# Kernel tuning notes

Hardware: AMD Instinct MI355X
Metric: run time of the kernel (lower is better)

## Reference

```python
import jax, jax.numpy as jnp
import numpy as np

N = 50000        # nodes
E = 800000       # edges (before self-loops)
IN = 128         # in_dim
H = 2            # heads
C1 = 64          # hidden_dim (per head)
D1 = H * C1      # conv1 concat output = 128
OUT = 64         # out_dim
C2 = 2 * OUT     # conv2 per-head channels = 128 (concat=False -> mean over heads)
NEG = 0.2        # GATv2 leaky_relu negative slope
EPS = 1e-5       # BatchNorm eps


def setup_inputs() -> dict:
    key = jax.random.key(0)
    ks = jax.random.split(key, 14)
    s = 0.05
    inp = {
        "x": jax.random.normal(ks[0], (N, IN), jnp.float32),
        "edge_index": jax.random.randint(ks[1], (2, E), 0, N, dtype=jnp.int32),
        # conv1 (GATv2: lin_l for source, lin_r for target, att vector per head)
        "W_l1": jax.random.normal(ks[2], (IN, D1), jnp.float32) * s,
        "b_l1": jnp.zeros((D1,), jnp.float32),
        "W_r1": jax.random.normal(ks[3], (IN, D1), jnp.float32) * s,
        "b_r1": jnp.zeros((D1,), jnp.float32),
        "att1": jax.random.normal(ks[4], (H, C1), jnp.float32) * s,
        "bias1": jnp.zeros((D1,), jnp.float32),
        # batch_norm1 (affine)
        "gamma1": jnp.ones((D1,), jnp.float32),
        "beta1": jnp.zeros((D1,), jnp.float32),
        # conv2
        "W_l2": jax.random.normal(ks[5], (D1, H * C2), jnp.float32) * s,
        "b_l2": jnp.zeros((H * C2,), jnp.float32),
        "W_r2": jax.random.normal(ks[6], (D1, H * C2), jnp.float32) * s,
        "b_r2": jnp.zeros((H * C2,), jnp.float32),
        "att2": jax.random.normal(ks[7], (H, C2), jnp.float32) * s,
        "bias2": jnp.zeros((C2,), jnp.float32),
    }
    return inp


def gatv2_layer(x, src, dst, W_l, b_l, W_r, b_r, att, bias, concat):
    Hh, Cc = att.shape
    x_l = (x @ W_l + b_l).reshape(N, Hh, Cc)   # source transform
    x_r = (x @ W_r + b_r).reshape(N, Hh, Cc)   # target transform
    # per-edge GATv2 score: att . leaky_relu(x_l[j] + x_r[i])
    e = jax.nn.leaky_relu(x_l[src] + x_r[dst], NEG)      # [E', H, C]
    logit = jnp.einsum("ehc,hc->eh", e, att)              # [E', H]
    # segment softmax over incoming edges of each target node
    m = jax.ops.segment_max(logit, dst, num_segments=N)   # [N, H]
    ex = jnp.exp(logit - m[dst])
    den = jax.ops.segment_sum(ex, dst, num_segments=N)    # [N, H]
    alpha = ex / den[dst]                                  # [E', H]
    out = jax.ops.segment_sum(x_l[src] * alpha[:, :, None], dst, num_segments=N)
    out = out.reshape(N, Hh * Cc) if concat else out.mean(axis=1)
    return out + bias


def batchnorm(x, gamma=None, beta=None):
    mu = x.mean(axis=0)
    var = x.var(axis=0)  # biased variance, as used by BN for normalization
    xn = (x - mu) * jax.lax.rsqrt(var + EPS)
    if gamma is not None:
        xn = xn * gamma + beta
    return xn


def reference(x, edge_index, W_l1, b_l1, W_r1, b_r1, att1, bias1, gamma1, beta1,
              W_l2, b_l2, W_r2, b_r2, att2, bias2):
    loops = jnp.arange(N, dtype=edge_index.dtype)
    src = jnp.concatenate([edge_index[0], loops])  # add self-loops (PyG default)
    dst = jnp.concatenate([edge_index[1], loops])
    h = gatv2_layer(x, src, dst, W_l1, b_l1, W_r1, b_r1, att1, bias1, True)
    h = jax.nn.relu(batchnorm(h, gamma1, beta1))
    o = gatv2_layer(h, src, dst, W_l2, b_l2, W_r2, b_r2, att2, bias2, False)
    mu_part = batchnorm(o[:, :OUT])                      # affine=False
    return jnp.concatenate([mu_part, jax.nn.softplus(o[:, OUT:])], axis=1)
```

## Files before the change

kernel.cpp:

```cpp
#include <hip/hip_runtime.h>
#include <hip/hip_bf16.h>
#include <math.h>

#define NNODES 50000
#define NEDGES 800000
#define EPTOT  (NEDGES + NNODES)
#define NEG_SLOPE 0.2f
#define BN_EPS 1e-5f
#define LOG2E 1.44269504088896f
#define ESLOT 64

#define PB_W1  128
#define PB_W2  (PB_W1 + 256)
#define GEMM1_GX 392
#define SCAT_BX  3321

typedef __hip_bfloat16 bf16;
typedef __attribute__((ext_vector_type(8))) short short8;
typedef __attribute__((ext_vector_type(4))) float f32x4;
typedef __attribute__((ext_vector_type(2))) float f32x2;

__device__ __forceinline__ unsigned short f2us(float f){
    return (unsigned short)(__bfloat16_as_ushort(__float2bfloat16(f)));
}
__device__ __forceinline__ f32x2 unpk(unsigned int w){
    union { unsigned int u; float f; } lo, hi;
    lo.u = w << 16; hi.u = w & 0xffff0000u;
    f32x2 r; r.x = lo.f; r.y = hi.f; return r;
}
__device__ __forceinline__ f32x2 pkmax(f32x2 a, f32x2 b){
#if __has_builtin(__builtin_elementwise_max)
    return __builtin_elementwise_max(a, b);
#else
    f32x2 r; r.x = fmaxf(a.x, b.x); r.y = fmaxf(a.y, b.y); return r;
#endif
}
__device__ __forceinline__ unsigned int pack2(float a, float b){
    return (unsigned int)f2us(a) | ((unsigned int)f2us(b) << 16);
}

template<int CTRL>
__device__ __forceinline__ float dppadd(float v){
    int p = __builtin_amdgcn_update_dpp(0, __float_as_int(v), CTRL, 0xf, 0xf, true);
    return v + __int_as_float(p);
}
template<int G>
__device__ __forceinline__ float group_sum(float v){
    if constexpr (G == 16){
        v = dppadd<0x121>(v);
        v = dppadd<0x122>(v);
        v = dppadd<0x124>(v);
        v = dppadd<0x128>(v);
    } else {
        v = dppadd<0xB1>(v);
        v = dppadd<0x4E>(v);
        v += __shfl_xor(v, 4, 64);
    }
    return v;
}


__global__ __launch_bounds__(256) void misc_prep(
    const float* __restrict__ Wl1, const float* __restrict__ Wr1,
    const float* __restrict__ bl1, const float* __restrict__ br1,
    bf16* __restrict__ WT1, float* __restrict__ bc1,
    const float* __restrict__ Wl2, const float* __restrict__ Wr2,
    const float* __restrict__ bl2, const float* __restrict__ br2,
    bf16* __restrict__ WT2, float* __restrict__ bc2)
{
    int b = blockIdx.x;
    if (b < PB_W1){
        int i = b * 256 + threadIdx.x;
        int r = i >> 7, k = i & 127;
        const float* W = (r < 128) ? Wl1 : Wr1;
        int c = (r < 128) ? r : r - 128;
        WT1[i] = __float2bfloat16(W[k * 128 + c]);
        if (k == 0) bc1[r] = (r < 128) ? bl1[c] : br1[c];
    } else {
        int i = (b - PB_W1) * 256 + threadIdx.x;
        int r = i >> 7, k = i & 127;
        const float* W = (r < 256) ? Wl2 : Wr2;
        int c = (r < 256) ? r : r - 256;
        WT2[i] = __float2bfloat16(W[k * 256 + c]);
        if (k == 0) bc2[r] = (r < 256) ? bl2[c] : br2[c];
    }
}


template<int DTOT, int AMODE, int NT, bool SCATTER>
__global__ __launch_bounds__(128) void mfma_gemm(
    const void* __restrict__ A, const bf16* __restrict__ WT,
    const float* __restrict__ biascat,
    bf16* __restrict__ xl, bf16* __restrict__ xr,
    const float* __restrict__ bns, const float* __restrict__ gamma,
    const float* __restrict__ beta,
    const int* __restrict__ ei, int* __restrict__ cnt, int* __restrict__ esrc)
{
    if (SCATTER && blockIdx.x >= GEMM1_GX){
        int e = ((blockIdx.x - GEMM1_GX) * 2 + blockIdx.y) * 128 + threadIdx.x;
        if (e < EPTOT){
            int s, d;
            if (e < NEDGES){ s = ei[e]; d = ei[NEDGES + e]; } else { s = d = e - NEDGES; }
            int pos = atomicAdd(&cnt[d], 1);
            if (pos < ESLOT) esrc[(d << 6) + pos] = s;
        }
        return;
    }

    int wave = threadIdx.x >> 6;
    int lane = threadIdx.x & 63;
    int quad = lane >> 4;
    int l16  = lane & 15;
    int m0 = blockIdx.x * 128 + wave * 64;
    const float* Af = (const float*)A;
    const unsigned int* Ao = (const unsigned int*)A;
    const short* Bp = (const short*)WT;

    short8 af[4][4];
    #pragma unroll
    for (int k = 0; k < 4; ++k){
        float sc[8], sh[8];
        if (AMODE == 2){
            const float inv_n = 1.f / (float)NNODES;
            int cb = k * 32 + quad * 8;
            #pragma unroll
            for (int j = 0; j < 8; ++j){
                float mu = bns[cb + j] * inv_n;
                float s  = gamma[cb + j] * rsqrtf(bns[128 + cb + j] * inv_n - mu * mu + BN_EPS);
                sc[j] = s; sh[j] = beta[cb + j] - mu * s;
            }
        }
        #pragma unroll
        for (int mt = 0; mt < 4; ++mt){
            int m = m0 + mt * 16 + l16;
            m = (m < NNODES) ? m : (NNODES - 1);
            if (AMODE == 1){
                float4 v0 = *(const float4*)(Af + (size_t)m * 128 + k * 32 + quad * 8);
                float4 v1 = *(const float4*)(Af + (size_t)m * 128 + k * 32 + quad * 8 + 4);
                unsigned int* u = (unsigned int*)&af[k][mt];
                u[0] = pack2(v0.x, v0.y); u[1] = pack2(v0.z, v0.w);
                u[2] = pack2(v1.x, v1.y); u[3] = pack2(v1.z, v1.w);
            } else {
                uint4 w = *(const uint4*)(Ao + (size_t)m * 64 + k * 16 + quad * 4);
                f32x2 v0 = unpk(w.x), v1 = unpk(w.y), v2 = unpk(w.z), v3 = unpk(w.w);
                float f0 = v0.x * sc[0] + sh[0], f1 = v0.y * sc[1] + sh[1];
                float f2 = v1.x * sc[2] + sh[2], f3 = v1.y * sc[3] + sh[3];
                float f4 = v2.x * sc[4] + sh[4], f5 = v2.y * sc[5] + sh[5];
                float f6 = v3.x * sc[6] + sh[6], f7 = v3.y * sc[7] + sh[7];
                f0 = f0 > 0.f ? f0 : 0.f; f1 = f1 > 0.f ? f1 : 0.f;
                f2 = f2 > 0.f ? f2 : 0.f; f3 = f3 > 0.f ? f3 : 0.f;
                f4 = f4 > 0.f ? f4 : 0.f; f5 = f5 > 0.f ? f5 : 0.f;
                f6 = f6 > 0.f ? f6 : 0.f; f7 = f7 > 0.f ? f7 : 0.f;
                unsigned int* u = (unsigned int*)&af[k][mt];
                u[0] = pack2(f0, f1); u[1] = pack2(f2, f3);
                u[2] = pack2(f4, f5); u[3] = pack2(f6, f7);
            }
        }
    }

    for (int t = 0; t < NT; ++t){
        int n0 = (blockIdx.y * NT + t) * 64;
        f32x4 acc[4][4] = {};
        #pragma unroll
        for (int k = 0; k < 4; ++k){
            short8 bfr[4];
            #pragma unroll
            for (int nt = 0; nt < 4; ++nt){
                int n = n0 + nt * 16 + l16;
                bfr[nt] = *(const short8*)(Bp + (size_t)n * 128 + k * 32 + quad * 8);
            }
            #pragma unroll
            for (int mt = 0; mt < 4; ++mt)
                #pragma unroll
                for (int nt = 0; nt < 4; ++nt)
                    acc[mt][nt] = __builtin_amdgcn_mfma_f32_16x16x32_bf16(af[k][mt], bfr[nt], acc[mt][nt], 0, 0, 0);
        }
        #pragma unroll
        for (int nt = 0; nt < 4; ++nt){
            int n = n0 + nt * 16 + l16;
            float bi = biascat[n];
            bf16* outp = (n < DTOT) ? xl : xr;
            int c = (n < DTOT) ? n : n - DTOT;
            #pragma unroll
            for (int mt = 0; mt < 4; ++mt)
                #pragma unroll
                for (int r = 0; r < 4; ++r){
                    int m = m0 + mt * 16 + quad * 4 + r;
                    if (m < NNODES)
                        outp[(size_t)m * DTOT + c] = __float2bfloat16(acc[mt][nt][r] + bi);
                }
        }
    }
}


template<int C, bool MEAN>
__global__ __launch_bounds__(256) void gat_aggregate(
    const bf16* __restrict__ xl, const bf16* __restrict__ xr,
    const float* __restrict__ att, const int* __restrict__ cnt,
    const int* __restrict__ esrc, void* __restrict__ outv,
    const float* __restrict__ bias2)
{
    constexpr int GH  = C / 8;
    constexpr int LPE = 2 * GH;
    constexpr int EL  = 64 / LPE;
    constexpr int RB  = 4 * C;
    int lane = threadIdx.x & 63;
    int wave = threadIdx.x >> 6;
    int n    = blockIdx.x * 4 + wave;
    int el   = lane / LPE;
    int h    = (lane / GH) & 1;
    int cl   = lane % GH;
    int rowoff = h * (C * 2) + cl * 16;
    const char* xlp = (const char*)xl;

    int srcAll = esrc[(n << 6) + lane];
    int cc = cnt[n];
    int c = (cc < ESLOT) ? cc : ESLOT;
    uint4 xw = *(const uint4*)((const char*)xr + (unsigned)n * RB + rowoff);
    f32x2 xr0 = unpk(xw.x), xr1 = unpk(xw.y), xr2v = unpk(xw.z), xr3 = unpk(xw.w);
    const float* ap = att + h * C + cl * 8;
    f32x2 av0 = {ap[0] * LOG2E, ap[1] * LOG2E};
    f32x2 av1 = {ap[2] * LOG2E, ap[3] * LOG2E};
    f32x2 av2 = {ap[4] * LOG2E, ap[5] * LOG2E};
    f32x2 av3 = {ap[6] * LOG2E, ap[7] * LOG2E};
    float b2r[8];
    if (MEAN){
        #pragma unroll
        for (int v = 0; v < 8; ++v) b2r[v] = bias2[cl * 8 + v];
    }

    float den = 0.f;
    f32x2 a0 = {0.f,0.f}, a1 = {0.f,0.f}, a2 = {0.f,0.f}, a3 = {0.f,0.f};

    int i0 = el, i1 = EL + el;
    int sa = __shfl(srcAll, (i0 < c) ? i0 : (c - 1), 64);
    int sb = __shfl(srcAll, (i1 < c) ? i1 : (c - 1), 64);
    uint4 wa = *(const uint4*)(xlp + ((unsigned)sa * (unsigned)RB + rowoff));
    uint4 wb = *(const uint4*)(xlp + ((unsigned)sb * (unsigned)RB + rowoff));

    int p = 0;
    for (; p + EL < c; p += 2 * EL){
        float mkb = (p + EL + el < c) ? 0.f : -1e30f;
        int pn = p + 2 * EL;
        uint4 wa_n, wb_n;
        bool pf = pn < c;
        if (pf){
            int ian = pn + el, ibn = pn + EL + el;
            int sa_n = __shfl(srcAll, (ian < c) ? ian : (c - 1), 64);
            int sb_n = __shfl(srcAll, (ibn < c) ? ibn : (c - 1), 64);
            wa_n = *(const uint4*)(xlp + ((unsigned)sa_n * (unsigned)RB + rowoff));
            wb_n = *(const uint4*)(xlp + ((unsigned)sb_n * (unsigned)RB + rowoff));
        }

        f32x2 xa0 = unpk(wa.x), xa1 = unpk(wa.y), xa2 = unpk(wa.z), xa3 = unpk(wa.w);
        f32x2 xb0 = unpk(wb.x), xb1 = unpk(wb.y), xb2 = unpk(wb.z), xb3 = unpk(wb.w);

        f32x2 ua0 = xa0 + xr0, ua1 = xa1 + xr1, ua2 = xa2 + xr2v, ua3 = xa3 + xr3;
        f32x2 ub0 = xb0 + xr0, ub1 = xb1 + xr1, ub2 = xb2 + xr2v, ub3 = xb3 + xr3;

        f32x2 ppa = pkmax(ua0, ua0 * NEG_SLOPE) * av0;
        ppa += pkmax(ua1, ua1 * NEG_SLOPE) * av1;
        ppa += pkmax(ua2, ua2 * NEG_SLOPE) * av2;
        ppa += pkmax(ua3, ua3 * NEG_SLOPE) * av3;
        f32x2 ppb = pkmax(ub0, ub0 * NEG_SLOPE) * av0;
        ppb += pkmax(ub1, ub1 * NEG_SLOPE) * av1;
        ppb += pkmax(ub2, ub2 * NEG_SLOPE) * av2;
        ppb += pkmax(ub3, ub3 * NEG_SLOPE) * av3;
        float parta = group_sum<GH>(ppa.x + ppa.y);
        float partb = group_sum<GH>(ppb.x + ppb.y);
        float exa = exp2f(parta);
        float exb = exp2f(partb + mkb);
        den += exa + exb;
        f32x2 ea = {exa, exa}, eb = {exb, exb};
        a0 += ea * xa0; a1 += ea * xa1; a2 += ea * xa2; a3 += ea * xa3;
        a0 += eb * xb0; a1 += eb * xb1; a2 += eb * xb2; a3 += eb * xb3;
        if (pf){ wa = wa_n; wb = wb_n; }
    }
    if (p < c){
        float mka = (p + el < c) ? 0.f : -1e30f;
        f32x2 xa0 = unpk(wa.x), xa1 = unpk(wa.y), xa2 = unpk(wa.z), xa3 = unpk(wa.w);
        f32x2 ua0 = xa0 + xr0, ua1 = xa1 + xr1, ua2 = xa2 + xr2v, ua3 = xa3 + xr3;

        f32x2 ppa = pkmax(ua0, ua0 * NEG_SLOPE) * av0;
        ppa += pkmax(ua1, ua1 * NEG_SLOPE) * av1;
        ppa += pkmax(ua2, ua2 * NEG_SLOPE) * av2;
        ppa += pkmax(ua3, ua3 * NEG_SLOPE) * av3;
        float parta = group_sum<GH>(ppa.x + ppa.y);
        float exa = exp2f(parta + mka);
        den += exa;
        f32x2 ea = {exa, exa};
        a0 += ea * xa0; a1 += ea * xa1; a2 += ea * xa2; a3 += ea * xa3;
    }

    #pragma unroll
    for (int mask = LPE; mask < 64; mask <<= 1){
        den  += __shfl_xor(den, mask, 64);
        a0.x += __shfl_xor(a0.x, mask, 64); a0.y += __shfl_xor(a0.y, mask, 64);
        a1.x += __shfl_xor(a1.x, mask, 64); a1.y += __shfl_xor(a1.y, mask, 64);
        a2.x += __shfl_xor(a2.x, mask, 64); a2.y += __shfl_xor(a2.y, mask, 64);
        a3.x += __shfl_xor(a3.x, mask, 64); a3.y += __shfl_xor(a3.y, mask, 64);
    }
    float inv = 1.f / den;

    if (!MEAN){
        if (el == 0){
            uint4 o;
            o.x = pack2(a0.x * inv, a0.y * inv);
            o.y = pack2(a1.x * inv, a1.y * inv);
            o.z = pack2(a2.x * inv, a2.y * inv);
            o.w = pack2(a3.x * inv, a3.y * inv);
            *(uint4*)((char*)outv + (size_t)n * RB + rowoff) = o;
        }
    } else {
        float v0 = a0.x * inv, v1 = a0.y * inv, v2 = a1.x * inv, v3 = a1.y * inv;
        float v4 = a2.x * inv, v5 = a2.y * inv, v6 = a3.x * inv, v7 = a3.y * inv;
        v0 = 0.5f * (v0 + __shfl_xor(v0, 16, 64)) + b2r[0];
        v1 = 0.5f * (v1 + __shfl_xor(v1, 16, 64)) + b2r[1];
        v2 = 0.5f * (v2 + __shfl_xor(v2, 16, 64)) + b2r[2];
        v3 = 0.5f * (v3 + __shfl_xor(v3, 16, 64)) + b2r[3];
        v4 = 0.5f * (v4 + __shfl_xor(v4, 16, 64)) + b2r[4];
        v5 = 0.5f * (v5 + __shfl_xor(v5, 16, 64)) + b2r[5];
        v6 = 0.5f * (v6 + __shfl_xor(v6, 16, 64)) + b2r[6];
        v7 = 0.5f * (v7 + __shfl_xor(v7, 16, 64)) + b2r[7];
        if (el == 0 && h == 0){
            float* outp = (float*)outv + (size_t)n * C + cl * 8;
            float4 w0 = {v0, v1, v2, v3};
            float4 w1 = {v4, v5, v6, v7};
            *(float4*)(outp) = w0;
            *(float4*)(outp + 4) = w1;
        }
    }
}


__global__ void bn_stats_bf16(const unsigned int* __restrict__ x, float* __restrict__ sums){
    __shared__ float ls[1024];
    int t = threadIdx.x;
    int c2 = t & 63;
    int rg = t >> 6;
    float s0 = 0.f, q0 = 0.f, s1 = 0.f, q1 = 0.f;
    for (int r = blockIdx.x * 4 + rg; r < NNODES; r += gridDim.x * 4){
        f32x2 v = unpk(x[(size_t)r * 64 + c2]);
        s0 += v.x; q0 += v.x * v.x;
        s1 += v.y; q1 += v.y * v.y;
    }
    ls[t] = s0; ls[256 + t] = q0; ls[512 + t] = s1; ls[768 + t] = q1;
    __syncthreads();
    if (rg == 0){
        for (int g = 1; g < 4; ++g){
            s0 += ls[g * 64 + c2];       q0 += ls[256 + g * 64 + c2];
            s1 += ls[512 + g * 64 + c2]; q1 += ls[768 + g * 64 + c2];
        }
        atomicAdd(&sums[2 * c2], s0);
        atomicAdd(&sums[128 + 2 * c2], q0);
        atomicAdd(&sums[2 * c2 + 1], s1);
        atomicAdd(&sums[128 + 2 * c2 + 1], q1);
    }
}

__global__ void bn_stats_o2(const float* __restrict__ x, float* __restrict__ sums){
    __shared__ float ls[512];
    int t = threadIdx.x;
    int col = t & 63;
    int rg  = t >> 6;
    float s = 0.f, q = 0.f;
    for (int r = blockIdx.x * 4 + rg; r < NNODES; r += gridDim.x * 4){
        float v = x[(size_t)r * 128 + col];
        s += v; q += v * v;
    }
    ls[t] = s; ls[256 + t] = q;
    __syncthreads();
    if (rg == 0){
        for (int g = 1; g < 4; ++g){ s += ls[g * 64 + col]; q += ls[256 + g * 64 + col]; }
        atomicAdd(&sums[col], s);
        atomicAdd(&sums[64 + col], q);
    }
}

__global__ void final_out(const float* __restrict__ o2, const float* __restrict__ sums,
                          float* __restrict__ out){
    int i = blockIdx.x * blockDim.x + threadIdx.x;
    if (i >= NNODES * 32) return;
    float4 v = *(const float4*)(o2 + (size_t)i * 4);
    int c = (i * 4) & 127;
    const float* vp = (const float*)&v;
    float4 r;
    float* rp = (float*)&r;
    if (c < 64){
        const float inv_n = 1.f / (float)NNODES;
        #pragma unroll
        for (int k = 0; k < 4; ++k){
            float mu = sums[c + k] * inv_n;
            float rsig = rsqrtf(sums[64 + c + k] * inv_n - mu * mu + BN_EPS);
            rp[k] = (vp[k] - mu) * rsig;
        }
    } else {
        #pragma unroll
        for (int k = 0; k < 4; ++k){
            float x = vp[k];
            rp[k] = (x > 20.f) ? x : log1pf(__expf(x));
        }
    }
    *(float4*)(out + (size_t)i * 4) = r;
}


extern "C" void kernel_launch(void* const* d_in, const int* in_sizes, int n_in,
                              void* d_out, int out_size, void* d_ws, size_t ws_size,
                              hipStream_t stream) {
    const float* x     = (const float*)d_in[0];
    const int*   ei    = (const int*)d_in[1];
    const float* W_l1  = (const float*)d_in[2];
    const float* b_l1  = (const float*)d_in[3];
    const float* W_r1  = (const float*)d_in[4];
    const float* b_r1  = (const float*)d_in[5];
    const float* att1  = (const float*)d_in[6];
    const float* gamma1 = (const float*)d_in[8];
    const float* beta1  = (const float*)d_in[9];
    const float* W_l2  = (const float*)d_in[10];
    const float* b_l2  = (const float*)d_in[11];
    const float* W_r2  = (const float*)d_in[12];
    const float* b_r2  = (const float*)d_in[13];
    const float* att2  = (const float*)d_in[14];
    const float* bias2 = (const float*)d_in[15];
    float* out = (float*)d_out;

    char* w = (char*)d_ws;
    size_t off = 0;
    auto alloc = [&](size_t bytes) -> void* {
        void* p = w + off;
        off += (bytes + 255) & ~(size_t)255;
        return p;
    };
    const size_t NF  = (size_t)NNODES * 128 * 4;
    bf16*  xl1   = (bf16*) alloc(NF / 2);
    bf16*  xr1   = (bf16*) alloc(NF / 2);
    bf16*  xl2   = (bf16*) alloc(NF);
    bf16*  xr2   = (bf16*) alloc(NF);
    unsigned int* o1 = (unsigned int*)alloc(NF / 2);
    float* o2    = (float*)alloc(NF);
    bf16*  WT1   = (bf16*) alloc(256 * 128 * 2);
    bf16*  WT2   = (bf16*) alloc(512 * 128 * 2);
    float* bc1   = (float*)alloc(256 * 4);
    float* bc2   = (float*)alloc(512 * 4);
    int*   cnt    = (int*)  alloc((size_t)NNODES * 4);
    int*   esrc   = (int*)  alloc((size_t)NNODES * ESLOT * 4);
    float* bnsums = (float*)alloc(384 * 4);
    float* bn1s = bnsums;
    float* bn2s = bnsums + 256;

    hipMemsetAsync(cnt, 0, (size_t)NNODES * 4, stream);
    hipMemsetAsync(bnsums, 0, 384 * 4, stream);

    misc_prep<<<PB_W2, 256, 0, stream>>>(W_l1, W_r1, b_l1, b_r1, WT1, bc1,
                                         W_l2, W_r2, b_l2, b_r2, WT2, bc2);

    mfma_gemm<128, 1, 2, true><<<dim3(GEMM1_GX + SCAT_BX, 2), 128, 0, stream>>>(
        x, WT1, bc1, xl1, xr1, nullptr, nullptr, nullptr, ei, cnt, esrc);
    gat_aggregate<64, false><<<NNODES / 4, 256, 0, stream>>>(xl1, xr1, att1, cnt, esrc, o1, bias2);

    bn_stats_bf16<<<512, 256, 0, stream>>>(o1, bn1s);

    mfma_gemm<256, 2, 2, false><<<dim3(392, 4), 128, 0, stream>>>(
        o1, WT2, bc2, xl2, xr2, bn1s, gamma1, beta1, nullptr, nullptr, nullptr);
    gat_aggregate<128, true><<<NNODES / 4, 256, 0, stream>>>(xl2, xr2, att2, cnt, esrc, o2, bias2);

    bn_stats_o2<<<512, 256, 0, stream>>>(o2, bn2s);
    final_out<<<(NNODES * 32 + 255) / 256, 256, 0, stream>>>(o2, bn2s, out);
}
```

Baseline: 386.6 us.

## Replace global-atomic edge bucketing with LDS histogram, prefix and placement passes

Edge bucketing by destination no longer uses one global atomicAdd per edge fused into the first GEMM launch. It now runs as three steps: per-chunk histograms in shared memory with two 16-bit counters packed per word (fused into misc_prep), a column-wise prefix over the 128 chunks, and a placement pass that does shared-memory atomics against the prefixed offsets. Source indices are stored as 16-bit values, which halves the esrc footprint read by both aggregation kernels. The cost is two extra launches and about 25 MB of histogram and offset traffic. The 16-bit source index is only valid because N is below 65536, and the per-chunk 16-bit counters assume no chunk overflows them.

```diff
diff --git a/kernel.cpp b/kernel.cpp
--- a/kernel.cpp
+++ b/kernel.cpp
@@ -12,8 +12,9 @@
 
 #define PB_W1  128
 #define PB_W2  (PB_W1 + 256)
-#define GEMM1_GX 392
-#define SCAT_BX  3321
+#define NSB    128
+#define SCHUNK ((EPTOT + NSB - 1) / NSB)
+#define NPAIR  (NNODES / 2)
 
 typedef __hip_bfloat16 bf16;
 typedef __attribute__((ext_vector_type(8))) short short8;
@@ -66,9 +67,26 @@
     bf16* __restrict__ WT1, float* __restrict__ bc1,
     const float* __restrict__ Wl2, const float* __restrict__ Wr2,
     const float* __restrict__ bl2, const float* __restrict__ br2,
-    bf16* __restrict__ WT2, float* __restrict__ bc2)
+    bf16* __restrict__ WT2, float* __restrict__ bc2,
+    const int* __restrict__ ei, unsigned int* __restrict__ ghist)
 {
+    __shared__ unsigned int hcnt[NPAIR];
     int b = blockIdx.x;
+    if (b >= PB_W2){
+        int g = b - PB_W2;
+        for (int i = threadIdx.x; i < NPAIR; i += 256) hcnt[i] = 0;
+        __syncthreads();
+        int e0 = g * SCHUNK;
+        int e1 = e0 + SCHUNK; if (e1 > EPTOT) e1 = EPTOT;
+        for (int e = e0 + threadIdx.x; e < e1; e += 256){
+            int d = (e < NEDGES) ? ei[NEDGES + e] : (e - NEDGES);
+            atomicAdd(&hcnt[d >> 1], (d & 1) ? 0x10000u : 1u);
+        }
+        __syncthreads();
+        for (int i = threadIdx.x; i < NPAIR; i += 256)
+            ghist[(size_t)g * NPAIR + i] = hcnt[i];
+        return;
+    }
     if (b < PB_W1){
         int i = b * 256 + threadIdx.x;
         int r = i >> 7, k = i & 127;
@@ -86,27 +104,54 @@
     }
 }
 
-
-template<int DTOT, int AMODE, int NT, bool SCATTER>
+__global__ void scat_prefix(const unsigned int* __restrict__ ghist,
+                            unsigned int* __restrict__ goff,
+                            int* __restrict__ cnt)
+{
+    int j = blockIdx.x * blockDim.x + threadIdx.x;
+    if (j >= NPAIR) return;
+    unsigned int lo = 0, hi = 0;
+    for (int g = 0; g < NSB; ++g){
+        unsigned int h = ghist[(size_t)g * NPAIR + j];
+        goff[(size_t)g * NPAIR + j] = lo | (hi << 16);
+        lo += h & 0xffffu;  hi += h >> 16;
+        lo = (lo > 0x3fffu) ? 0x3fffu : lo;
+        hi = (hi > 0x3fffu) ? 0x3fffu : hi;
+    }
+    int2 v; v.x = (int)lo; v.y = (int)hi;
+    *(int2*)(cnt + 2 * j) = v;
+}
+
+__global__ __launch_bounds__(256) void scat_place(
+    const int* __restrict__ ei, const unsigned int* __restrict__ goff,
+    unsigned short* __restrict__ esrc)
+{
+    __shared__ unsigned int pcnt[NPAIR];
+    int g = blockIdx.x;
+    for (int i = threadIdx.x; i < NPAIR; i += 256)
+        pcnt[i] = goff[(size_t)g * NPAIR + i];
+    __syncthreads();
+    int e0 = g * SCHUNK;
+    int e1 = e0 + SCHUNK; if (e1 > EPTOT) e1 = EPTOT;
+    for (int e = e0 + threadIdx.x; e < e1; e += 256){
+        int s, d;
+        if (e < NEDGES){ s = ei[e]; d = ei[NEDGES + e]; }
+        else           { s = d = e - NEDGES; }
+        unsigned int old = atomicAdd(&pcnt[d >> 1], (d & 1) ? 0x10000u : 1u);
+        unsigned int slot = (d & 1) ? (old >> 16) : (old & 0xffffu);
+        if (slot < ESLOT) esrc[((unsigned)d << 6) + slot] = (unsigned short)s;
+    }
+}
+
+
+template<int DTOT, int AMODE, int NT>
 __global__ __launch_bounds__(128) void mfma_gemm(
     const void* __restrict__ A, const bf16* __restrict__ WT,
     const float* __restrict__ biascat,
     bf16* __restrict__ xl, bf16* __restrict__ xr,
     const float* __restrict__ bns, const float* __restrict__ gamma,
-    const float* __restrict__ beta,
-    const int* __restrict__ ei, int* __restrict__ cnt, int* __restrict__ esrc)
+    const float* __restrict__ beta)
 {
-    if (SCATTER && blockIdx.x >= GEMM1_GX){
-        int e = ((blockIdx.x - GEMM1_GX) * 2 + blockIdx.y) * 128 + threadIdx.x;
-        if (e < EPTOT){
-            int s, d;
-            if (e < NEDGES){ s = ei[e]; d = ei[NEDGES + e]; } else { s = d = e - NEDGES; }
-            int pos = atomicAdd(&cnt[d], 1);
-            if (pos < ESLOT) esrc[(d << 6) + pos] = s;
-        }
-        return;
-    }
-
     int wave = threadIdx.x >> 6;
     int lane = threadIdx.x & 63;
     int quad = lane >> 4;
@@ -198,7 +243,7 @@
 __global__ __launch_bounds__(256) void gat_aggregate(
     const bf16* __restrict__ xl, const bf16* __restrict__ xr,
     const float* __restrict__ att, const int* __restrict__ cnt,
-    const int* __restrict__ esrc, void* __restrict__ outv,
+    const unsigned short* __restrict__ esrc, void* __restrict__ outv,
     const float* __restrict__ bias2)
 {
     constexpr int GH  = C / 8;
@@ -214,7 +259,7 @@
     int rowoff = h * (C * 2) + cl * 16;
     const char* xlp = (const char*)xl;
 
-    int srcAll = esrc[(n << 6) + lane];
+    int srcAll = (int)esrc[(n << 6) + lane];
     int cc = cnt[n];
     int c = (cc < ESLOT) ? cc : ESLOT;
     uint4 xw = *(const uint4*)((const char*)xr + (unsigned)n * RB + rowoff);
@@ -445,25 +490,29 @@
     float* bc1   = (float*)alloc(256 * 4);
     float* bc2   = (float*)alloc(512 * 4);
     int*   cnt    = (int*)  alloc((size_t)NNODES * 4);
-    int*   esrc   = (int*)  alloc((size_t)NNODES * ESLOT * 4);
+    unsigned short* esrc = (unsigned short*)alloc((size_t)NNODES * ESLOT * 2);
+    unsigned int* ghist  = (unsigned int*)alloc((size_t)NSB * NPAIR * 4);
+    unsigned int* goff   = (unsigned int*)alloc((size_t)NSB * NPAIR * 4);
     float* bnsums = (float*)alloc(384 * 4);
     float* bn1s = bnsums;
     float* bn2s = bnsums + 256;
 
-    hipMemsetAsync(cnt, 0, (size_t)NNODES * 4, stream);
     hipMemsetAsync(bnsums, 0, 384 * 4, stream);
 
-    misc_prep<<<PB_W2, 256, 0, stream>>>(W_l1, W_r1, b_l1, b_r1, WT1, bc1,
-                                         W_l2, W_r2, b_l2, b_r2, WT2, bc2);
-
-    mfma_gemm<128, 1, 2, true><<<dim3(GEMM1_GX + SCAT_BX, 2), 128, 0, stream>>>(
-        x, WT1, bc1, xl1, xr1, nullptr, nullptr, nullptr, ei, cnt, esrc);
+    misc_prep<<<PB_W2 + NSB, 256, 0, stream>>>(W_l1, W_r1, b_l1, b_r1, WT1, bc1,
+                                               W_l2, W_r2, b_l2, b_r2, WT2, bc2,
+                                               ei, ghist);
+    scat_prefix<<<(NPAIR + 255) / 256, 256, 0, stream>>>(ghist, goff, cnt);
+    scat_place<<<NSB, 256, 0, stream>>>(ei, goff, esrc);
+
+    mfma_gemm<128, 1, 2><<<dim3(392, 2), 128, 0, stream>>>(
+        x, WT1, bc1, xl1, xr1, nullptr, nullptr, nullptr);
     gat_aggregate<64, false><<<NNODES / 4, 256, 0, stream>>>(xl1, xr1, att1, cnt, esrc, o1, bias2);
 
     bn_stats_bf16<<<512, 256, 0, stream>>>(o1, bn1s);
 
-    mfma_gemm<256, 2, 2, false><<<dim3(392, 4), 128, 0, stream>>>(
-        o1, WT2, bc2, xl2, xr2, bn1s, gamma1, beta1, nullptr, nullptr, nullptr);
+    mfma_gemm<256, 2, 2><<<dim3(392, 4), 128, 0, stream>>>(
+        o1, WT2, bc2, xl2, xr2, bn1s, gamma1, beta1);
     gat_aggregate<128, true><<<NNODES / 4, 256, 0, stream>>>(xl2, xr2, att2, cnt, esrc, o2, bias2);
 
     bn_stats_o2<<<512, 256, 0, stream>>>(o2, bn2s);
```

New measurement: 405.3 us. 4.8% more time.
